# Performance work log

Hardware: AMD Instinct MI355X
Metric: run time of the kernel (lower is better)

## Reference

```python
import jax, jax.numpy as jnp
import numpy as np

N_NODES = 100000
N_EDGES = 1600000
IN_CH = 128
HID = 64
HEADS = 2
OUT_CH = 2
EDGE_DIM = 3
NEG_SLOPE = 0.2
EPS = 1e-16  # PyG softmax denominator epsilon


def gat_conv(x, edge_index, edge_attr, W, We, att_src, att_dst, att_edge, bias, heads, out_ch, concat):
    """Faithful PyG GATConv (edge_dim enabled, eval mode, add_self_loops handled by caller=False here
    since the repo passes raw edge_index; PyG default add_self_loops=True is intentionally mirrored below)."""
    N = x.shape[0]
    src, dst = edge_index[0], edge_index[1]
    H, C = heads, out_ch
    h = (x @ W).reshape(N, H, C)                    # [N,H,C] node projections
    e = (edge_attr @ We).reshape(-1, H, C)          # [E,H,C] edge projections
    a_src = jnp.sum(h * att_src, axis=-1)           # [N,H]
    a_dst = jnp.sum(h * att_dst, axis=-1)           # [N,H]
    alpha = a_src[src] + a_dst[dst] + jnp.sum(e * att_edge, axis=-1)  # [E,H]
    alpha = jax.nn.leaky_relu(alpha, NEG_SLOPE)
    # segment softmax over incoming edges of each dst node
    amax = jax.ops.segment_max(alpha, dst, num_segments=N)            # [N,H]
    amax = jnp.where(jnp.isfinite(amax), amax, 0.0)
    alpha = jnp.exp(alpha - amax[dst])
    denom = jax.ops.segment_sum(alpha, dst, num_segments=N)           # [N,H]
    alpha = alpha / (denom[dst] + EPS)
    msg = h[src] * alpha[:, :, None]                                  # [E,H,C]
    out = jax.ops.segment_sum(msg, dst, num_segments=N)               # [N,H,C]
    if concat:
        out = out.reshape(N, H * C)
    else:
        out = out.mean(axis=1)
    return out + bias


def add_self_loops(edge_index, edge_attr, n):
    loops = jnp.arange(n, dtype=edge_index.dtype)
    ei = jnp.concatenate([edge_index, jnp.stack([loops, loops])], axis=1)
    ea = jnp.concatenate([edge_attr, jnp.zeros((n, edge_attr.shape[1]), edge_attr.dtype)], axis=0)
    return ei, ea


def setup_inputs() -> dict:
    key = jax.random.key(0)
    ks = jax.random.split(key, 16)
    s = 0.1
    x = jax.random.normal(ks[0], (N_NODES, IN_CH), jnp.float32)
    edge_index = jax.random.randint(ks[1], (2, N_EDGES), 0, N_NODES, jnp.int64 if jax.config.jax_enable_x64 else jnp.int32)
    edge_feat = jax.random.normal(ks[2], (N_EDGES, EDGE_DIM), jnp.float32)
    HC = HEADS * HID
    return {
        "x": x, "edge_index": edge_index, "edge_feat": edge_feat,
        "W1": jax.random.normal(ks[3], (IN_CH, HC), jnp.float32) * s,
        "We1": jax.random.normal(ks[4], (EDGE_DIM, HC), jnp.float32) * s,
        "as1": jax.random.normal(ks[5], (1, HEADS, HID), jnp.float32) * s,
        "ad1": jax.random.normal(ks[6], (1, HEADS, HID), jnp.float32) * s,
        "ae1": jax.random.normal(ks[7], (1, HEADS, HID), jnp.float32) * s,
        "b1": jnp.zeros((HC,), jnp.float32),
        "W2": jax.random.normal(ks[8], (HC, OUT_CH), jnp.float32) * s,
        "We2": jax.random.normal(ks[9], (EDGE_DIM, OUT_CH), jnp.float32) * s,
        "as2": jax.random.normal(ks[10], (1, 1, OUT_CH), jnp.float32) * s,
        "ad2": jax.random.normal(ks[11], (1, 1, OUT_CH), jnp.float32) * s,
        "ae2": jax.random.normal(ks[12], (1, 1, OUT_CH), jnp.float32) * s,
        "b2": jnp.zeros((OUT_CH,), jnp.float32),
    }


def reference(x, edge_index, edge_feat, W1, We1, as1, ad1, ae1, b1, W2, We2, as2, ad2, ae2, b2):
    # eval mode: F.dropout is identity
    ei, ea = add_self_loops(edge_index, edge_feat, x.shape[0])  # PyG GATConv default add_self_loops=True
    h = gat_conv(x, ei, ea, W1, We1, as1, ad1, ae1, b1, HEADS, HID, concat=True)
    h = jax.nn.elu(h)
    out = gat_conv(h, ei, ea, W2, We2, as2, ad2, ae2, b2, 1, OUT_CH, concat=False)
    return out
```

## Files before the change

kernel.cpp:

```cpp
#include <hip/hip_runtime.h>
#include <hip/hip_bf16.h>

#define NN 100000
#define NE 1600000
#define NEG_SLOPE 0.2f
#define GEPS 1e-16f

typedef __attribute__((ext_vector_type(8))) short short8;
typedef __attribute__((ext_vector_type(4))) float f32x4;

__device__ __forceinline__ unsigned short f2b(float f) {
  unsigned u = __float_as_uint(f);
  u += 0x7fffu + ((u >> 16) & 1u);
  return (unsigned short)(u >> 16);
}
__device__ __forceinline__ float blo(unsigned u) { return __uint_as_float(u << 16); }
__device__ __forceinline__ float bhi(unsigned u) { return __uint_as_float(u & 0xffff0000u); }

__global__ void k_prep(const float* __restrict__ We1, const float* __restrict__ ae1,
                       const float* __restrict__ We2, const float* __restrict__ ae2,
                       const float* __restrict__ W1, const float* __restrict__ as1,
                       const float* __restrict__ ad1,
                       float* __restrict__ q, float4* __restrict__ pq) {
  int t = threadIdx.x;
  if (t < 6) {
    int d = t >> 1, hh = t & 1;
    float s = 0.f;
    for (int c = 0; c < 64; ++c) s += We1[d * 128 + hh * 64 + c] * ae1[hh * 64 + c];
    q[t] = s;
  } else if (t < 9) {
    int d = t - 6;
    q[8 + d] = We2[d * 2 + 0] * ae2[0] + We2[d * 2 + 1] * ae2[1];
  }
  if (t < 128) {
    float s0 = 0.f, s1 = 0.f, d0 = 0.f, d1 = 0.f;
    for (int c = 0; c < 64; ++c) {
      float w0 = W1[t * 128 + c], w1 = W1[t * 128 + 64 + c];
      s0 += w0 * as1[c];      s1 += w1 * as1[64 + c];
      d0 += w0 * ad1[c];      d1 += w1 * ad1[64 + c];
    }
    pq[t] = make_float4(s0, s1, d0, d1);
  }
}

__global__ __launch_bounds__(512, 4) void k_gemm(const float* __restrict__ x,
                                                 const float* __restrict__ W,
                                                 const float4* __restrict__ pq,
                                                 unsigned short* __restrict__ h1b,
                                                 float* __restrict__ a1s,
                                                 float* __restrict__ a1d) {
  __shared__ unsigned short xa[128 * 128];
  __shared__ unsigned short wt[128 * 128];
  int t = threadIdx.x;
  int row0 = blockIdx.x * 128;

  {
    int kr = t >> 2, n0 = (t & 3) * 32;
    const float* wp = &W[kr * 128 + n0];
    int cb = kr >> 3, klo = kr & 7;
#pragma unroll
    for (int j = 0; j < 8; ++j) {
      float4 v = *(const float4*)&wp[j * 4];
      int n = n0 + j * 4;
      wt[(n + 0) * 128 + ((cb ^ ((n + 0) & 15)) * 8) + klo] = f2b(v.x);
      wt[(n + 1) * 128 + ((cb ^ ((n + 1) & 15)) * 8) + klo] = f2b(v.y);
      wt[(n + 2) * 128 + ((cb ^ ((n + 2) & 15)) * 8) + klo] = f2b(v.z);
      wt[(n + 3) * 128 + ((cb ^ ((n + 3) & 15)) * 8) + klo] = f2b(v.w);
    }
  }
  {
    int lrow = t >> 2, qq = t & 3;
    int grow = row0 + lrow; if (grow >= NN) grow = NN - 1;
    const float* xp = &x[(size_t)grow * 128 + qq * 32];
    const float4* pqp = &pq[qq * 32];
    float ps0 = 0.f, ps1 = 0.f, pd0 = 0.f, pd1 = 0.f;
    int sw = lrow & 15;
#pragma unroll
    for (int j = 0; j < 4; ++j) {
      float4 u = *(const float4*)&xp[j * 8];
      float4 v = *(const float4*)&xp[j * 8 + 4];
      float xs[8] = {u.x, u.y, u.z, u.w, v.x, v.y, v.z, v.w};
      short8 sv;
#pragma unroll
      for (int e = 0; e < 8; ++e) {
        float4 pv = pqp[j * 8 + e];
        ps0 += xs[e] * pv.x; ps1 += xs[e] * pv.y;
        pd0 += xs[e] * pv.z; pd1 += xs[e] * pv.w;
        sv[e] = (short)f2b(xs[e]);
      }
      int c = qq * 4 + j;
      *(short8*)&xa[lrow * 128 + ((c ^ sw) * 8)] = sv;
    }
    ps0 += __shfl_xor(ps0, 1); ps0 += __shfl_xor(ps0, 2);
    ps1 += __shfl_xor(ps1, 1); ps1 += __shfl_xor(ps1, 2);
    pd0 += __shfl_xor(pd0, 1); pd0 += __shfl_xor(pd0, 2);
    pd1 += __shfl_xor(pd1, 1); pd1 += __shfl_xor(pd1, 2);
    if (qq == 0) {
      *(float2*)&a1s[grow * 2] = make_float2(ps0, ps1);
      *(float2*)&a1d[grow * 2] = make_float2(pd0, pd1);
    }
  }
  __syncthreads();

  int lane = t & 63, w = t >> 6;
  int m = lane & 15, quad = lane >> 4;
  int wm = (w & 1) * 64, wn = (w >> 1) * 32;
  f32x4 acc[4][2];
#pragma unroll
  for (int mi = 0; mi < 4; ++mi)
#pragma unroll
    for (int ni = 0; ni < 2; ++ni) acc[mi][ni] = (f32x4)(0.f);

#pragma unroll
  for (int kk = 0; kk < 4; ++kk) {
    int c = kk * 4 + quad;
    int co = (c ^ m) * 8;
    short8 a[4], b[2];
#pragma unroll
    for (int mi = 0; mi < 4; ++mi)
      a[mi] = *(const short8*)&xa[(wm + mi * 16 + m) * 128 + co];
#pragma unroll
    for (int ni = 0; ni < 2; ++ni)
      b[ni] = *(const short8*)&wt[(wn + ni * 16 + m) * 128 + co];
#pragma unroll
    for (int mi = 0; mi < 4; ++mi)
#pragma unroll
      for (int ni = 0; ni < 2; ++ni)
        acc[mi][ni] = __builtin_amdgcn_mfma_f32_16x16x32_bf16(a[mi], b[ni], acc[mi][ni], 0, 0, 0);
  }
#pragma unroll
  for (int mi = 0; mi < 4; ++mi)
#pragma unroll
    for (int r = 0; r < 4; ++r) {
      int grow = row0 + wm + mi * 16 + quad * 4 + r;
      if (grow >= NN) grow = NN - 1;
#pragma unroll
      for (int ni = 0; ni < 2; ++ni)
        h1b[(size_t)grow * 128 + wn + ni * 16 + m] = f2b(acc[mi][ni][r]);
    }
}

__global__ void k_hist(const int* __restrict__ ei, int* __restrict__ deg,
                       int* __restrict__ rank) {
  int t4 = blockIdx.x * 256 + threadIdx.x;
  if (t4 >= NE / 4) return;
  int4 d = *(const int4*)&ei[NE + t4 * 4];
  int4 rk;
  rk.x = atomicAdd(&deg[d.x], 1);
  rk.y = atomicAdd(&deg[d.y], 1);
  rk.z = atomicAdd(&deg[d.z], 1);
  rk.w = atomicAdd(&deg[d.w], 1);
  *(int4*)&rank[t4 * 4] = rk;
}

__device__ __forceinline__ int padlen(int d) { return (d + 8) & ~7; }

__global__ void k_scan1(const int* __restrict__ deg, int* __restrict__ bsum) {
  __shared__ int lds[256];
  int t = threadIdx.x;
  int base = blockIdx.x * 1024 + t * 4;
  int s = 0;
  for (int j = 0; j < 4; ++j) { int i = base + j; s += (i < NN) ? padlen(deg[i]) : 0; }
  lds[t] = s; __syncthreads();
  for (int o = 128; o > 0; o >>= 1) { if (t < o) lds[t] += lds[t + o]; __syncthreads(); }
  if (t == 0) bsum[blockIdx.x] = lds[0];
}

__global__ void k_scan2(int* __restrict__ bsum, int nb) {
  __shared__ int lds[128];
  int t = threadIdx.x;
  int v = (t < nb) ? bsum[t] : 0;
  lds[t] = v; __syncthreads();
  for (int o = 1; o < 128; o <<= 1) {
    int u = (t >= o) ? lds[t - o] : 0;
    __syncthreads();
    lds[t] += u;
    __syncthreads();
  }
  if (t < nb) bsum[t] = lds[t] - v;
}

__global__ void k_scan3(const int* __restrict__ deg, const int* __restrict__ bbase,
                        const float* __restrict__ a1s, const float* __restrict__ a1d,
                        int* __restrict__ rowptr, float4* __restrict__ cpk) {
  __shared__ int lds[256];
  int t = threadIdx.x;
  int base = blockIdx.x * 1024 + t * 4;
  int v[4]; int s = 0;
  for (int j = 0; j < 4; ++j) { int i = base + j; v[j] = (i < NN) ? padlen(deg[i]) : 0; s += v[j]; }
  lds[t] = s; __syncthreads();
  for (int o = 1; o < 256; o <<= 1) {
    int u = (t >= o) ? lds[t - o] : 0;
    __syncthreads();
    lds[t] += u;
    __syncthreads();
  }
  int excl = lds[t] - s + bbase[blockIdx.x];
  for (int j = 0; j < 4; ++j) {
    int i = base + j;
    if (i <= NN) rowptr[i] = excl;
    if (i < NN) {
      float al0 = a1s[i * 2] + a1d[i * 2];
      float al1 = a1s[i * 2 + 1] + a1d[i * 2 + 1];
      al0 = al0 > 0.f ? al0 : NEG_SLOPE * al0;
      al1 = al1 > 0.f ? al1 : NEG_SLOPE * al1;
      float4 pk;
      pk.x = __expf(al0); pk.y = __expf(al1);
      pk.z = __int_as_float(i); pk.w = 0.f;
      cpk[excl] = pk;
      float4 pad;
      pad.x = 0.f; pad.y = 0.f; pad.z = __int_as_float(i); pad.w = -1e30f;
      for (int k = 1 + deg[i]; k < v[j]; ++k) cpk[excl + k] = pad;
    }
    excl += v[j];
  }
}

__global__ void k_scatter(const int* __restrict__ ei, const float* __restrict__ ef,
                          const float* __restrict__ a1s, const float* __restrict__ a1d,
                          const float* __restrict__ q, const int* __restrict__ rowptr,
                          const int* __restrict__ rank, float4* __restrict__ cpk) {
  int t4 = blockIdx.x * 256 + threadIdx.x;
  if (t4 >= NE / 4) return;
  int e0 = t4 * 4;
  int4 ss = *(const int4*)&ei[e0];
  int4 dd = *(const int4*)&ei[NE + e0];
  int4 rk = *(const int4*)&rank[e0];
  float4 fA = *(const float4*)&ef[e0 * 3];
  float4 fB = *(const float4*)&ef[e0 * 3 + 4];
  float4 fC = *(const float4*)&ef[e0 * 3 + 8];
  float f[4][3] = {{fA.x, fA.y, fA.z}, {fA.w, fB.x, fB.y},
                   {fB.z, fB.w, fC.x}, {fC.y, fC.z, fC.w}};
  int src[4] = {ss.x, ss.y, ss.z, ss.w};
  int dst[4] = {dd.x, dd.y, dd.z, dd.w};
  int rnk[4] = {rk.x, rk.y, rk.z, rk.w};
#pragma unroll
  for (int j = 0; j < 4; ++j) {
    float e0h = f[j][0] * q[0] + f[j][1] * q[2] + f[j][2] * q[4];
    float e1h = f[j][0] * q[1] + f[j][1] * q[3] + f[j][2] * q[5];
    float ez  = f[j][0] * q[8] + f[j][1] * q[9] + f[j][2] * q[10];
    float al0 = a1s[src[j] * 2] + a1d[dst[j] * 2] + e0h;
    float al1 = a1s[src[j] * 2 + 1] + a1d[dst[j] * 2 + 1] + e1h;
    al0 = al0 > 0.f ? al0 : NEG_SLOPE * al0;
    al1 = al1 > 0.f ? al1 : NEG_SLOPE * al1;
    int pos = rowptr[dst[j]] + 1 + rnk[j];
    float4 pk;
    pk.x = __expf(al0); pk.y = __expf(al1);
    pk.z = __int_as_float(src[j]); pk.w = ez;
    cpk[pos] = pk;
  }
}

__global__ __launch_bounds__(256) void k_agg1(const unsigned short* __restrict__ h1b,
                                              const int* __restrict__ rowptr,
                                              const float4* __restrict__ cpk,
                                              const float* __restrict__ b1,
                                              const float* __restrict__ W2,
                                              const float* __restrict__ as2,
                                              const float* __restrict__ ad2,
                                              float4* __restrict__ nd) {
  int n = (int)((blockIdx.x * 256 + threadIdx.x) >> 6);
  int lane = threadIdx.x & 63;
  if (n >= NN) return;
  int s0 = rowptr[n], s1 = rowptr[n + 1];
  int g = lane >> 4;
  int lp = lane & 15;
  bool head1 = lp >= 8;

  float acc[8];
#pragma unroll
  for (int j = 0; j < 8; ++j) acc[j] = 0.f;
  float den = 0.f;

  int i = s0;
  for (; i + 16 <= s1; i += 16) {
    float4 pA = cpk[i + g], pB = cpk[i + 4 + g], pC = cpk[i + 8 + g], pD = cpk[i + 12 + g];
    uint4 vA = *((const uint4*)(h1b + ((size_t)__float_as_int(pA.z) << 7)) + lp);
    uint4 vB = *((const uint4*)(h1b + ((size_t)__float_as_int(pB.z) << 7)) + lp);
    uint4 vC = *((const uint4*)(h1b + ((size_t)__float_as_int(pC.z) << 7)) + lp);
    uint4 vD = *((const uint4*)(h1b + ((size_t)__float_as_int(pD.z) << 7)) + lp);
    float eA = head1 ? pA.y : pA.x;
    float eB = head1 ? pB.y : pB.x;
    float eC = head1 ? pC.y : pC.x;
    float eD = head1 ? pD.y : pD.x;
    den += (eA + eB) + (eC + eD);
    acc[0] += eA * blo(vA.x) + eB * blo(vB.x) + eC * blo(vC.x) + eD * blo(vD.x);
    acc[1] += eA * bhi(vA.x) + eB * bhi(vB.x) + eC * bhi(vC.x) + eD * bhi(vD.x);
    acc[2] += eA * blo(vA.y) + eB * blo(vB.y) + eC * blo(vC.y) + eD * blo(vD.y);
    acc[3] += eA * bhi(vA.y) + eB * bhi(vB.y) + eC * bhi(vC.y) + eD * bhi(vD.y);
    acc[4] += eA * blo(vA.z) + eB * blo(vB.z) + eC * blo(vC.z) + eD * blo(vD.z);
    acc[5] += eA * bhi(vA.z) + eB * bhi(vB.z) + eC * bhi(vC.z) + eD * bhi(vD.z);
    acc[6] += eA * blo(vA.w) + eB * blo(vB.w) + eC * blo(vC.w) + eD * blo(vD.w);
    acc[7] += eA * bhi(vA.w) + eB * bhi(vB.w) + eC * bhi(vC.w) + eD * bhi(vD.w);
  }
  if (i < s1) {
    float4 pA = cpk[i + g], pB = cpk[i + 4 + g];
    uint4 vA = *((const uint4*)(h1b + ((size_t)__float_as_int(pA.z) << 7)) + lp);
    uint4 vB = *((const uint4*)(h1b + ((size_t)__float_as_int(pB.z) << 7)) + lp);
    float eA = head1 ? pA.y : pA.x;
    float eB = head1 ? pB.y : pB.x;
    den += eA + eB;
    acc[0] += eA * blo(vA.x) + eB * blo(vB.x);
    acc[1] += eA * bhi(vA.x) + eB * bhi(vB.x);
    acc[2] += eA * blo(vA.y) + eB * blo(vB.y);
    acc[3] += eA * bhi(vA.y) + eB * bhi(vB.y);
    acc[4] += eA * blo(vA.z) + eB * blo(vB.z);
    acc[5] += eA * bhi(vA.z) + eB * bhi(vB.z);
    acc[6] += eA * blo(vA.w) + eB * blo(vB.w);
    acc[7] += eA * bhi(vA.w) + eB * bhi(vB.w);
  }
#pragma unroll
  for (int o = 16; o <= 32; o <<= 1) {
    den += __shfl_xor(den, o);
#pragma unroll
    for (int j = 0; j < 8; ++j) acc[j] += __shfl_xor(acc[j], o);
  }
  float4 bA = *(const float4*)&b1[lp * 8];
  float4 bB = *(const float4*)&b1[lp * 8 + 4];
  float bb[8] = {bA.x, bA.y, bA.z, bA.w, bB.x, bB.y, bB.z, bB.w};
  float inv = 1.f / (den + GEPS);
  float r[8];
#pragma unroll
  for (int j = 0; j < 8; ++j) {
    float v = acc[j] * inv + bb[j];
    r[j] = v > 0.f ? v : __expf(v) - 1.f;
  }
  float4 wA = *(const float4*)&W2[lp * 16];
  float4 wB = *(const float4*)&W2[lp * 16 + 4];
  float4 wC = *(const float4*)&W2[lp * 16 + 8];
  float4 wD = *(const float4*)&W2[lp * 16 + 12];
  float p20 = r[0] * wA.x + r[1] * wA.z + r[2] * wB.x + r[3] * wB.z
            + r[4] * wC.x + r[5] * wC.z + r[6] * wD.x + r[7] * wD.z;
  float p21 = r[0] * wA.y + r[1] * wA.w + r[2] * wB.y + r[3] * wB.w
            + r[4] * wC.y + r[5] * wC.w + r[6] * wD.y + r[7] * wD.w;
#pragma unroll
  for (int o = 1; o <= 8; o <<= 1) { p20 += __shfl_xor(p20, o); p21 += __shfl_xor(p21, o); }
  if (lane == 0) {
    float4 v;
    v.x = p20; v.y = p21;
    v.z = p20 * as2[0] + p21 * as2[1];
    v.w = p20 * ad2[0] + p21 * ad2[1];
    nd[n] = v;
  }
}

__global__ __launch_bounds__(256) void k_agg2(const int* __restrict__ rowptr,
                                              const float4* __restrict__ cpk,
                                              const float4* __restrict__ nd,
                                              const float* __restrict__ b2,
                                              float* __restrict__ out) {
  int wid = (int)((blockIdx.x * 256 + threadIdx.x) >> 6);
  int lane = threadIdx.x & 63;
  int g = lane >> 4, lp = lane & 15;
  int n = wid * 4 + g;
  if (n >= NN) return;
  int s0 = rowptr[n], s1 = rowptr[n + 1];
  float adn = nd[n].w;
  float den = 0.f, acc0 = 0.f, acc1 = 0.f;
  for (int i = s0 + lp; i < s1; i += 16) {
    float4 pk = cpk[i];
    int s = __float_as_int(pk.z);
    float4 ns = nd[s];
    float v = ns.z + adn + pk.w;
    v = v > 0.f ? v : NEG_SLOPE * v;
    float p = __expf(v);
    den += p;
    acc0 += p * ns.x;
    acc1 += p * ns.y;
  }
#pragma unroll
  for (int o = 1; o <= 8; o <<= 1) {
    den += __shfl_xor(den, o);
    acc0 += __shfl_xor(acc0, o);
    acc1 += __shfl_xor(acc1, o);
  }
  if (lp == 0) {
    float2 r;
    r.x = acc0 / (den + GEPS) + b2[0];
    r.y = acc1 / (den + GEPS) + b2[1];
    *(float2*)&out[n * 2] = r;
  }
}

extern "C" void kernel_launch(void* const* d_in, const int* in_sizes, int n_in,
                              void* d_out, int out_size, void* d_ws, size_t ws_size,
                              hipStream_t stream) {
  (void)in_sizes; (void)n_in; (void)out_size; (void)ws_size;
  const float* x   = (const float*)d_in[0];
  const int*   ei  = (const int*)d_in[1];
  const float* ef  = (const float*)d_in[2];
  const float* W1  = (const float*)d_in[3];
  const float* We1 = (const float*)d_in[4];
  const float* as1 = (const float*)d_in[5];
  const float* ad1 = (const float*)d_in[6];
  const float* ae1 = (const float*)d_in[7];
  const float* b1  = (const float*)d_in[8];
  const float* W2  = (const float*)d_in[9];
  const float* We2 = (const float*)d_in[10];
  const float* as2 = (const float*)d_in[11];
  const float* ad2 = (const float*)d_in[12];
  const float* ae2 = (const float*)d_in[13];
  const float* b2  = (const float*)d_in[14];
  float* out = (float*)d_out;

  char* w = (char*)d_ws;
  auto alloc = [&](size_t bytes) -> char* {
    char* p = w; w += (bytes + 255) & ~(size_t)255; return p;
  };
  unsigned short* h1b = (unsigned short*)alloc((size_t)NN * 128 * 2);
  float*  a1s    = (float*)alloc((size_t)NN * 2 * 4);
  float*  a1d    = (float*)alloc((size_t)NN * 2 * 4);
  float4* nd     = (float4*)alloc((size_t)NN * 16);
  float*  q      = (float*)alloc(64);
  float4* pq     = (float4*)alloc(128 * 16);
  int*    deg    = (int*)alloc((size_t)NN * 4);
  int*    rowptr = (int*)alloc((size_t)(NN + 1) * 4);
  int*    rank   = (int*)alloc((size_t)NE * 4);
  int*    bsum   = (int*)alloc(128 * 4);
  float4* cpk    = (float4*)alloc(((size_t)NE + 8 * NN) * 16);

  const int NB_SCAN = (NN + 1023) / 1024;

  hipLaunchKernelGGL(k_prep, dim3(1), dim3(128), 0, stream,
                     We1, ae1, We2, ae2, W1, as1, ad1, q, pq);
  hipLaunchKernelGGL(k_gemm, dim3((NN + 127) / 128), dim3(512), 0, stream,
                     x, W1, pq, h1b, a1s, a1d);
  hipMemsetAsync(deg, 0, (size_t)NN * 4, stream);
  hipLaunchKernelGGL(k_hist, dim3((NE / 4 + 255) / 256), dim3(256), 0, stream, ei, deg, rank);
  hipLaunchKernelGGL(k_scan1, dim3(NB_SCAN), dim3(256), 0, stream, deg, bsum);
  hipLaunchKernelGGL(k_scan2, dim3(1), dim3(128), 0, stream, bsum, NB_SCAN);
  hipLaunchKernelGGL(k_scan3, dim3(NB_SCAN), dim3(256), 0, stream,
                     deg, bsum, a1s, a1d, rowptr, cpk);
  hipLaunchKernelGGL(k_scatter, dim3((NE / 4 + 255) / 256), dim3(256), 0, stream,
                     ei, ef, a1s, a1d, q, rowptr, rank, cpk);
  hipLaunchKernelGGL(k_agg1, dim3((NN * 64 + 255) / 256), dim3(256), 0, stream,
                     h1b, rowptr, cpk, b1, W2, as2, ad2, nd);
  hipLaunchKernelGGL(k_agg2, dim3(((NN + 3) / 4 * 64 + 255) / 256), dim3(256), 0, stream,
                     rowptr, cpk, nd, b2, out);
}
```

Measured before the change: 388.1 us.

## Switch layer-1 aggregation to fp16 packed dot2 with shifted exp weights

Stores h1 in fp16 instead of bf16 and packs the two per-head softmax weights as fp16 pairs, shifted by a constant to avoid overflow. The aggregation inner loop uses v_dot2 fp16 instructions with byte-permutes to pair edges, cutting the VALU instruction count per edge roughly in half. The cpk layout is rearranged so the edge term moves into .y. This trades some precision (fp16 range and accuracy of exp weights) for fewer arithmetic instructions in a kernel that may be memory-bound.

```diff
diff --git a/kernel.cpp b/kernel.cpp
--- a/kernel.cpp
+++ b/kernel.cpp
@@ -5,17 +5,33 @@
 #define NE 1600000
 #define NEG_SLOPE 0.2f
 #define GEPS 1e-16f
+#define WSHIFT 4.0f
 
 typedef __attribute__((ext_vector_type(8))) short short8;
 typedef __attribute__((ext_vector_type(4))) float f32x4;
+typedef __attribute__((ext_vector_type(2))) _Float16 h2v;
 
 __device__ __forceinline__ unsigned short f2b(float f) {
   unsigned u = __float_as_uint(f);
   u += 0x7fffu + ((u >> 16) & 1u);
   return (unsigned short)(u >> 16);
 }
-__device__ __forceinline__ float blo(unsigned u) { return __uint_as_float(u << 16); }
-__device__ __forceinline__ float bhi(unsigned u) { return __uint_as_float(u & 0xffff0000u); }
+__device__ __forceinline__ unsigned short f2h(float f) {
+  _Float16 h = (_Float16)f;
+  return __builtin_bit_cast(unsigned short, h);
+}
+__device__ __forceinline__ unsigned pkh2(float lo, float hi) {
+  return (unsigned)f2h(lo) | ((unsigned)f2h(hi) << 16);
+}
+__device__ __forceinline__ float dot2h(unsigned a, unsigned b, float c) {
+  return __builtin_amdgcn_fdot2(__builtin_bit_cast(h2v, a), __builtin_bit_cast(h2v, b), c, false);
+}
+__device__ __forceinline__ unsigned permb(unsigned s0, unsigned s1, int sel) {
+  return __builtin_amdgcn_perm(s0, s1, sel);
+}
+#define HSEL_LO 0x05040100
+#define HSEL_HI 0x07060302
+#define ONE2    0x3C003C00u
 
 __global__ void k_prep(const float* __restrict__ We1, const float* __restrict__ ae1,
                        const float* __restrict__ We2, const float* __restrict__ ae2,
@@ -136,7 +152,7 @@
       if (grow >= NN) grow = NN - 1;
 #pragma unroll
       for (int ni = 0; ni < 2; ++ni)
-        h1b[(size_t)grow * 128 + wn + ni * 16 + m] = f2b(acc[mi][ni][r]);
+        h1b[(size_t)grow * 128 + wn + ni * 16 + m] = f2h(acc[mi][ni][r]);
     }
 }
 
@@ -205,11 +221,11 @@
       al0 = al0 > 0.f ? al0 : NEG_SLOPE * al0;
       al1 = al1 > 0.f ? al1 : NEG_SLOPE * al1;
       float4 pk;
-      pk.x = __expf(al0); pk.y = __expf(al1);
-      pk.z = __int_as_float(i); pk.w = 0.f;
+      pk.x = __uint_as_float(pkh2(__expf(al0 - WSHIFT), __expf(al1 - WSHIFT)));
+      pk.y = 0.f; pk.z = __int_as_float(i); pk.w = 0.f;
       cpk[excl] = pk;
       float4 pad;
-      pad.x = 0.f; pad.y = 0.f; pad.z = __int_as_float(i); pad.w = -1e30f;
+      pad.x = 0.f; pad.y = -1e30f; pad.z = __int_as_float(i); pad.w = 0.f;
       for (int k = 1 + deg[i]; k < v[j]; ++k) cpk[excl + k] = pad;
     }
     excl += v[j];
@@ -245,8 +261,8 @@
     al1 = al1 > 0.f ? al1 : NEG_SLOPE * al1;
     int pos = rowptr[dst[j]] + 1 + rnk[j];
     float4 pk;
-    pk.x = __expf(al0); pk.y = __expf(al1);
-    pk.z = __int_as_float(src[j]); pk.w = ez;
+    pk.x = __uint_as_float(pkh2(__expf(al0 - WSHIFT), __expf(al1 - WSHIFT)));
+    pk.y = ez; pk.z = __int_as_float(src[j]); pk.w = 0.f;
     cpk[pos] = pk;
   }
 }
@@ -265,7 +281,7 @@
   int s0 = rowptr[n], s1 = rowptr[n + 1];
   int g = lane >> 4;
   int lp = lane & 15;
-  bool head1 = lp >= 8;
+  int wsel = (lp >= 8) ? HSEL_HI : HSEL_LO;
 
   float acc[8];
 #pragma unroll
@@ -279,35 +295,41 @@
     uint4 vB = *((const uint4*)(h1b + ((size_t)__float_as_int(pB.z) << 7)) + lp);
     uint4 vC = *((const uint4*)(h1b + ((size_t)__float_as_int(pC.z) << 7)) + lp);
     uint4 vD = *((const uint4*)(h1b + ((size_t)__float_as_int(pD.z) << 7)) + lp);
-    float eA = head1 ? pA.y : pA.x;
-    float eB = head1 ? pB.y : pB.x;
-    float eC = head1 ? pC.y : pC.x;
-    float eD = head1 ? pD.y : pD.x;
-    den += (eA + eB) + (eC + eD);
-    acc[0] += eA * blo(vA.x) + eB * blo(vB.x) + eC * blo(vC.x) + eD * blo(vD.x);
-    acc[1] += eA * bhi(vA.x) + eB * bhi(vB.x) + eC * bhi(vC.x) + eD * bhi(vD.x);
-    acc[2] += eA * blo(vA.y) + eB * blo(vB.y) + eC * blo(vC.y) + eD * blo(vD.y);
-    acc[3] += eA * bhi(vA.y) + eB * bhi(vB.y) + eC * bhi(vC.y) + eD * bhi(vD.y);
-    acc[4] += eA * blo(vA.z) + eB * blo(vB.z) + eC * blo(vC.z) + eD * blo(vD.z);
-    acc[5] += eA * bhi(vA.z) + eB * bhi(vB.z) + eC * bhi(vC.z) + eD * bhi(vD.z);
-    acc[6] += eA * blo(vA.w) + eB * blo(vB.w) + eC * blo(vC.w) + eD * blo(vD.w);
-    acc[7] += eA * bhi(vA.w) + eB * bhi(vB.w) + eC * bhi(vC.w) + eD * bhi(vD.w);
+    unsigned wAB = permb(__float_as_uint(pB.x), __float_as_uint(pA.x), wsel);
+    unsigned wCD = permb(__float_as_uint(pD.x), __float_as_uint(pC.x), wsel);
+    den = dot2h(wAB, ONE2, den);
+    den = dot2h(wCD, ONE2, den);
+    acc[0] = dot2h(permb(vB.x, vA.x, HSEL_LO), wAB, acc[0]);
+    acc[1] = dot2h(permb(vB.x, vA.x, HSEL_HI), wAB, acc[1]);
+    acc[2] = dot2h(permb(vB.y, vA.y, HSEL_LO), wAB, acc[2]);
+    acc[3] = dot2h(permb(vB.y, vA.y, HSEL_HI), wAB, acc[3]);
+    acc[4] = dot2h(permb(vB.z, vA.z, HSEL_LO), wAB, acc[4]);
+    acc[5] = dot2h(permb(vB.z, vA.z, HSEL_HI), wAB, acc[5]);
+    acc[6] = dot2h(permb(vB.w, vA.w, HSEL_LO), wAB, acc[6]);
+    acc[7] = dot2h(permb(vB.w, vA.w, HSEL_HI), wAB, acc[7]);
+    acc[0] = dot2h(permb(vD.x, vC.x, HSEL_LO), wCD, acc[0]);
+    acc[1] = dot2h(permb(vD.x, vC.x, HSEL_HI), wCD, acc[1]);
+    acc[2] = dot2h(permb(vD.y, vC.y, HSEL_LO), wCD, acc[2]);
+    acc[3] = dot2h(permb(vD.y, vC.y, HSEL_HI), wCD, acc[3]);
+    acc[4] = dot2h(permb(vD.z, vC.z, HSEL_LO), wCD, acc[4]);
+    acc[5] = dot2h(permb(vD.z, vC.z, HSEL_HI), wCD, acc[5]);
+    acc[6] = dot2h(permb(vD.w, vC.w, HSEL_LO), wCD, acc[6]);
+    acc[7] = dot2h(permb(vD.w, vC.w, HSEL_HI), wCD, acc[7]);
   }
   if (i < s1) {
     float4 pA = cpk[i + g], pB = cpk[i + 4 + g];
     uint4 vA = *((const uint4*)(h1b + ((size_t)__float_as_int(pA.z) << 7)) + lp);
     uint4 vB = *((const uint4*)(h1b + ((size_t)__float_as_int(pB.z) << 7)) + lp);
-    float eA = head1 ? pA.y : pA.x;
-    float eB = head1 ? pB.y : pB.x;
-    den += eA + eB;
-    acc[0] += eA * blo(vA.x) + eB * blo(vB.x);
-    acc[1] += eA * bhi(vA.x) + eB * bhi(vB.x);
-    acc[2] += eA * blo(vA.y) + eB * blo(vB.y);
-    acc[3] += eA * bhi(vA.y) + eB * bhi(vB.y);
-    acc[4] += eA * blo(vA.z) + eB * blo(vB.z);
-    acc[5] += eA * bhi(vA.z) + eB * bhi(vB.z);
-    acc[6] += eA * blo(vA.w) + eB * blo(vB.w);
-    acc[7] += eA * bhi(vA.w) + eB * bhi(vB.w);
+    unsigned wAB = permb(__float_as_uint(pB.x), __float_as_uint(pA.x), wsel);
+    den = dot2h(wAB, ONE2, den);
+    acc[0] = dot2h(permb(vB.x, vA.x, HSEL_LO), wAB, acc[0]);
+    acc[1] = dot2h(permb(vB.x, vA.x, HSEL_HI), wAB, acc[1]);
+    acc[2] = dot2h(permb(vB.y, vA.y, HSEL_LO), wAB, acc[2]);
+    acc[3] = dot2h(permb(vB.y, vA.y, HSEL_HI), wAB, acc[3]);
+    acc[4] = dot2h(permb(vB.z, vA.z, HSEL_LO), wAB, acc[4]);
+    acc[5] = dot2h(permb(vB.z, vA.z, HSEL_HI), wAB, acc[5]);
+    acc[6] = dot2h(permb(vB.w, vA.w, HSEL_LO), wAB, acc[6]);
+    acc[7] = dot2h(permb(vB.w, vA.w, HSEL_HI), wAB, acc[7]);
   }
 #pragma unroll
   for (int o = 16; o <= 32; o <<= 1) {
@@ -361,7 +383,7 @@
     float4 pk = cpk[i];
     int s = __float_as_int(pk.z);
     float4 ns = nd[s];
-    float v = ns.z + adn + pk.w;
+    float v = ns.z + adn + pk.y;
     v = v > 0.f ? v : NEG_SLOPE * v;
     float p = __expf(v);
     den += p;
```

Measured after the change: 386.3 us. No clear change (-0.5%).
